# Performance work log

Hardware: AMD Instinct MI355X
Metric: run time of the kernel (lower is better)

Reference implementation:

```python
import jax, jax.numpy as jnp
import numpy as np

B, S, E = 2, 2048, 1024
H, D = 16, 64  # NUM_ATTENTION_HEADS, NUM_FEATURES
LN_EPS = 1e-5


def setup_inputs() -> dict:
    key = jax.random.key(0)
    ks = jax.random.split(key, 10)
    scale = 1.0 / np.sqrt(E)
    return {
        "x": jax.random.normal(ks[0], (B, S, E), dtype=jnp.float32),
        "ln_g": jnp.ones((E,), dtype=jnp.float32),
        "ln_b": jnp.zeros((E,), dtype=jnp.float32),
        "wq": jax.random.normal(ks[1], (E, H * D), dtype=jnp.float32) * scale,
        "bq": jnp.zeros((H * D,), dtype=jnp.float32),
        "wk": jax.random.normal(ks[2], (E, H * D), dtype=jnp.float32) * scale,
        "bk": jnp.zeros((H * D,), dtype=jnp.float32),
        "wv": jax.random.normal(ks[3], (E, H * D), dtype=jnp.float32) * scale,
        "bv": jnp.zeros((H * D,), dtype=jnp.float32),
        "wo": jax.random.normal(ks[4], (H * D, E), dtype=jnp.float32) * scale,
        "bo": jnp.zeros((E,), dtype=jnp.float32),
    }


def reference(x, ln_g, ln_b, wq, bq, wk, bk, wv, bv, wo, bo):
    x_residual = x
    # LayerNorm over last dim
    mean = jnp.mean(x, axis=-1, keepdims=True)
    var = jnp.mean(jnp.square(x - mean), axis=-1, keepdims=True)
    xn = (x - mean) * jax.lax.rsqrt(var + LN_EPS) * ln_g + ln_b

    q = (xn @ wq + bq).reshape(B, S, H, D)
    k = (xn @ wk + bk).reshape(B, S, H, D)
    v = (xn @ wv + bv).reshape(B, S, H, D)

    # scores: [B, S_q, S_k, H]
    score = jnp.einsum('bihd,bjhd->bijh', q, k) / np.sqrt(D).astype(np.float32)
    # causal mask: position i may not attend to j > i
    causal = jnp.tril(jnp.ones((S, S), dtype=bool))  # True = keep
    score = jnp.where(causal[None, :, :, None], score, -jnp.inf)
    probs = jax.nn.softmax(score, axis=2)

    out = jnp.einsum('bijh,bjhd->bihd', probs, v).reshape(B, S, H * D)
    out = out @ wo + bo
    return out + x_residual
```

## Files before the change

### kernel.cpp

```cpp
#include <hip/hip_runtime.h>
#include <math.h>
#include <stdint.h>

typedef short short8 __attribute__((ext_vector_type(8)));
typedef short s16x4 __attribute__((ext_vector_type(4)));
typedef float f32x4 __attribute__((ext_vector_type(4)));

constexpr int BB = 2, SS = 2048, EE = 1024, HH = 16, DD = 64, HD = 1024;
constexpr int NROW = BB * SS;
constexpr size_t WELEM = (size_t)1024 * 1024;
constexpr float LN_EPS = 1e-5f;

__device__ const int ENT_QT[40] = {0,1,2,3, 4,4, 5,5, 6,6, 7,7,
                                   8,8,8, 9,9,9, 10,10,10, 11,11,11,
                                   12,12,12,12, 13,13,13,13, 14,14,14,14, 15,15,15,15};
__device__ const int ENT_C0[40] = {0,0,0,0, 0,1, 0,1, 0,1, 0,1,
                                   0,1,2, 0,1,2, 0,1,2, 0,1,2,
                                   0,1,2,3, 0,1,2,3, 0,1,2,3, 0,1,2,3};
__device__ const int EBASE[16]  = {0,1,2,3,4,6,8,10,12,15,18,21,24,28,32,36};
constexpr int NENT = 40;

__device__ inline short f2bf(float f) {
    union { float f; uint32_t u; } v; v.f = f;
    uint32_t r = (v.u + 0x7fffu + ((v.u >> 16) & 1u)) >> 16;
    return (short)(uint16_t)r;
}

__device__ inline float bf2f(short s) {
    return __uint_as_float(((uint32_t)(uint16_t)s) << 16);
}

__device__ inline uint32_t pk2bf(float f0, float f1) {
    uint32_t u0 = __float_as_uint(f0) + 0x8000u;
    uint32_t u1 = __float_as_uint(f1) + 0x8000u;
    return __builtin_amdgcn_perm(u1, u0, 0x07060302u);
}

__device__ inline s16x4 pack_bf16x4(f32x4 v) {
    union { uint32_t u[2]; s16x4 s; } r;
    r.u[0] = pk2bf(v[0], v[1]);
    r.u[1] = pk2bf(v[2], v[3]);
    return r.s;
}

#define GLOBAL_TO_LDS16(g, l) \
    __builtin_amdgcn_global_load_lds( \
        (const __attribute__((address_space(1))) void*)(g), \
        (__attribute__((address_space(3))) void*)(l), 16, 0, 0)

__global__ void prep_kernel(const float* __restrict__ x,
                            const float* __restrict__ g,
                            const float* __restrict__ b,
                            short* __restrict__ xn,
                            const float* __restrict__ w0, const float* __restrict__ w1,
                            const float* __restrict__ w2, const float* __restrict__ w3,
                            short* __restrict__ wdst) {
    const int bx = blockIdx.x;
    const int t = threadIdx.x;
    if (bx < NROW) {
        const int row = bx;
        const float* xr = x + (size_t)row * EE;
        short* onr = xn + (size_t)row * EE;
        float4 v = ((const float4*)xr)[t];
        float s  = v.x + v.y + v.z + v.w;
        float ss = v.x * v.x + v.y * v.y + v.z * v.z + v.w * v.w;
        #pragma unroll
        for (int o = 32; o > 0; o >>= 1) {
            s  += __shfl_down(s, o);
            ss += __shfl_down(ss, o);
        }
        __shared__ float sm[4], sm2[4];
        const int wid = t >> 6, lane = t & 63;
        if (lane == 0) { sm[wid] = s; sm2[wid] = ss; }
        __syncthreads();
        float ts  = sm[0] + sm[1] + sm[2] + sm[3];
        float tss = sm2[0] + sm2[1] + sm2[2] + sm2[3];
        float mean = ts * (1.0f / EE);
        float var  = tss * (1.0f / EE) - mean * mean;
        float inv  = rsqrtf(var + LN_EPS);
        float4 gv = ((const float4*)g)[t];
        float4 bv = ((const float4*)b)[t];
        s16x4 st;
        st.x = f2bf((v.x - mean) * inv * gv.x + bv.x);
        st.y = f2bf((v.y - mean) * inv * gv.y + bv.y);
        st.z = f2bf((v.z - mean) * inv * gv.z + bv.z);
        st.w = f2bf((v.w - mean) * inv * gv.w + bv.w);
        ((s16x4*)onr)[t] = st;
    } else {
        const int widx = bx - NROW;
        const int z = widx >> 10;
        const int rem = widx & 1023;
        const int k0 = (rem >> 5) * 32, p0 = (rem & 31) * 32;
        const float* src = (z == 0) ? w0 : (z == 1) ? w1 : (z == 2) ? w2 : w3;
        short* d = wdst + (size_t)z * WELEM;
        __shared__ float tile[32][33];
        const int tx = t & 31, ty = t >> 5;
        #pragma unroll
        for (int r = ty; r < 32; r += 8)
            tile[r][tx] = src[(size_t)(k0 + r) * 1024 + p0 + tx];
        __syncthreads();
        #pragma unroll
        for (int r = ty; r < 32; r += 8)
            d[(size_t)(p0 + r) * 1024 + k0 + tx] = f2bf(tile[tx][r]);
    }
}

template <bool F32OUT>
__global__ __launch_bounds__(256) void mfma_gemm(
    const short* __restrict__ A,
    const short* __restrict__ BtBase,
    const float* __restrict__ b0, const float* __restrict__ b1,
    const float* __restrict__ b2,
    short* __restrict__ outB, short* __restrict__ outV,
    const float* __restrict__ resid, float* __restrict__ outF) {
    constexpr int K = 1024, N = 1024;
    const int t = threadIdx.x, lane = t & 63, w = t >> 6;
    const int quad = lane >> 4, l16 = lane & 15;
    const int wm = w >> 1, wn = w & 1;
    const int row0 = blockIdx.y * 128, col0 = blockIdx.x * 128;
    const int z = blockIdx.z;
    const short* Bt = BtBase + (size_t)z * WELEM;
    const float* bias = (z == 0) ? b0 : (z == 1) ? b1 : b2;

    __shared__ short As[128 * 32];
    __shared__ short Bs[128 * 32];

    f32x4 acc[4][4];
    #pragma unroll
    for (int i = 0; i < 4; i++)
        #pragma unroll
        for (int j = 0; j < 4; j++) acc[i][j] = (f32x4){0.f, 0.f, 0.f, 0.f};

    const int srow = t >> 2, schunk = t & 3;
    const short* agp = A  + (size_t)(row0 + srow) * K + schunk * 8;
    const short* bgp = Bt + (size_t)(col0 + srow) * K + schunk * 8;

    for (int k0 = 0; k0 < K; k0 += 32) {
        GLOBAL_TO_LDS16(agp + k0,                    As + t * 8);
        GLOBAL_TO_LDS16(agp + (size_t)64 * K + k0,   As + 2048 + t * 8);
        GLOBAL_TO_LDS16(bgp + k0,                    Bs + t * 8);
        GLOBAL_TO_LDS16(bgp + (size_t)64 * K + k0,   Bs + 2048 + t * 8);
        __syncthreads();
        short8 af[4], bf[4];
        #pragma unroll
        for (int mt = 0; mt < 4; mt++)
            af[mt] = *(const short8*)&As[(wm * 64 + mt * 16 + l16) * 32 + quad * 8];
        #pragma unroll
        for (int nt = 0; nt < 4; nt++)
            bf[nt] = *(const short8*)&Bs[(wn * 64 + nt * 16 + l16) * 32 + quad * 8];
        #pragma unroll
        for (int mt = 0; mt < 4; mt++)
            #pragma unroll
            for (int nt = 0; nt < 4; nt++)
                acc[mt][nt] = __builtin_amdgcn_mfma_f32_16x16x32_bf16(
                    af[mt], bf[nt], acc[mt][nt], 0, 0, 0);
        __syncthreads();
    }

    #pragma unroll
    for (int mt = 0; mt < 4; mt++) {
        #pragma unroll
        for (int nt = 0; nt < 4; nt++) {
            const int rbase = row0 + wm * 64 + mt * 16 + quad * 4;
            const int col = col0 + wn * 64 + nt * 16 + l16;
            const float bcol = bias[col];
            if (F32OUT) {
                #pragma unroll
                for (int r = 0; r < 4; r++)
                    outF[(size_t)(rbase + r) * N + col] =
                        acc[mt][nt][r] + bcol +
                        resid[(size_t)(rbase + r) * N + col];
            } else if (z == 2) {
                union { uint32_t u[2]; s16x4 s; } pk;
                pk.u[0] = pk2bf(acc[mt][nt][0] + bcol, acc[mt][nt][1] + bcol);
                pk.u[1] = pk2bf(acc[mt][nt][2] + bcol, acc[mt][nt][3] + bcol);
                *(s16x4*)&outV[(size_t)col * NROW + rbase] = pk.s;
            } else {
                #pragma unroll
                for (int r = 0; r < 4; r++)
                    outB[(size_t)z * NROW * N + (size_t)(rbase + r) * N + col] =
                        f2bf(acc[mt][nt][r] + bcol);
            }
        }
    }
}

__global__ __launch_bounds__(256) void attn_split(
    const short* __restrict__ q, const short* __restrict__ kkk,
    const short* __restrict__ vtp,
    short* __restrict__ OpartB, float* __restrict__ lpart) {
    const int e = NENT - 1 - (int)blockIdx.x;
    const int h = blockIdx.y, b = blockIdx.z;
    const int qt = ENT_QT[e], c0 = ENT_C0[e];
    const int t = threadIdx.x, lane = t & 63, w = t >> 6;
    const int quad = lane >> 4, l16 = lane & 15;
    const int sw = l16 & 7;
    const int i0 = qt * 128;

    __shared__ short Qs[128 * 64];
    __shared__ short Kb[2 * 64 * 64];
    __shared__ short Vb[2 * 64 * 64];

    const size_t qoff = ((size_t)(b * SS + i0)) * HD + h * DD;
    #pragma unroll
    for (int p = 0; p < 4; p++) {
        const int idx = t + p * 256;
        const int r = idx >> 3, cs = idx & 7;
        const int c = cs ^ (r & 7);
        GLOBAL_TO_LDS16(q + qoff + (size_t)r * HD + c * 8, Qs + idx * 8);
    }

    const int r0 = t >> 3,        cs0 = t & 7;
    const int r1 = (t + 256) >> 3, cs1 = (t + 256) & 7;
    const short* kb0 = kkk + ((size_t)b * SS) * HD + h * DD + (size_t)r0 * HD + (cs0 ^ (r0 & 7)) * 8;
    const short* kb1 = kkk + ((size_t)b * SS) * HD + h * DD + (size_t)r1 * HD + (cs1 ^ (r1 & 7)) * 8;
    const short* vb0 = vtp + ((size_t)(h * 64 + r0)) * NROW + b * SS + (cs0 ^ (r0 & 7)) * 8;
    const short* vb1 = vtp + ((size_t)(h * 64 + r1)) * NROW + b * SS + (cs1 ^ (r1 & 7)) * 8;

    f32x4 Ot[4][2];
    float lrun[2] = {0.f, 0.f};
    #pragma unroll
    for (int mtd = 0; mtd < 4; mtd++)
        #pragma unroll
        for (int nt = 0; nt < 2; nt++) Ot[mtd][nt] = (f32x4){0.f, 0.f, 0.f, 0.f};

    const int jt0 = c0 * 8;
    const int jt1 = min(jt0 + 8, 2 * qt + 2);

    {
        const size_t ko = (size_t)jt0 * 64 * HD;
        const int vo = jt0 * 64;
        GLOBAL_TO_LDS16(kb0 + ko, Kb + t * 8);
        GLOBAL_TO_LDS16(kb1 + ko, Kb + (t + 256) * 8);
        GLOBAL_TO_LDS16(vb0 + vo, Vb + t * 8);
        GLOBAL_TO_LDS16(vb1 + vo, Vb + (t + 256) * 8);
    }
    __syncthreads();

    int buf = 0;
    for (int jt = jt0; jt < jt1; ++jt) {
        if (jt + 1 < jt1) {
            const size_t ko = (size_t)(jt + 1) * 64 * HD;
            const int vo = (jt + 1) * 64;
            const int ob = (buf ^ 1) * 4096;
            GLOBAL_TO_LDS16(kb0 + ko, Kb + ob + t * 8);
            GLOBAL_TO_LDS16(kb1 + ko, Kb + ob + (t + 256) * 8);
            GLOBAL_TO_LDS16(vb0 + vo, Vb + ob + t * 8);
            GLOBAL_TO_LDS16(vb1 + vo, Vb + ob + (t + 256) * 8);
        }
        const short* Kc = Kb + buf * 4096;
        const short* Vc = Vb + buf * 4096;

        f32x4 s[4][2];
        #pragma unroll
        for (int mj = 0; mj < 4; mj++)
            #pragma unroll
            for (int nt = 0; nt < 2; nt++) s[mj][nt] = (f32x4){0.f, 0.f, 0.f, 0.f};
        #pragma unroll
        for (int ks = 0; ks < 2; ks++) {
            const int cq = ((ks * 4 + quad) ^ sw) * 8;
            short8 kf[4], qf[2];
            #pragma unroll
            for (int mj = 0; mj < 4; mj++)
                kf[mj] = *(const short8*)&Kc[(mj * 16 + l16) * 64 + cq];
            #pragma unroll
            for (int nt = 0; nt < 2; nt++)
                qf[nt] = *(const short8*)&Qs[(w * 32 + nt * 16 + l16) * 64 + cq];
            #pragma unroll
            for (int mj = 0; mj < 4; mj++)
                #pragma unroll
                for (int nt = 0; nt < 2; nt++)
                    s[mj][nt] = __builtin_amdgcn_mfma_f32_16x16x32_bf16(
                        kf[mj], qf[nt], s[mj][nt], 0, 0, 0);
        }

        const bool diag = (jt >= 2 * qt);
        const int joff = (jt - 2 * qt) * 64;
        const int irel = w * 32 + l16;
        #pragma unroll
        for (int mj = 0; mj < 4; mj++) {
            #pragma unroll
            for (int nt = 0; nt < 2; nt++) {
                const int ir = irel + nt * 16;
                #pragma unroll
                for (int r = 0; r < 4; r++) {
                    const int jrel = joff + mj * 16 + quad * 4 + r;
                    float p = exp2f(s[mj][nt][r] * 0.18033688f);
                    if (diag && (jrel > ir)) p = 0.f;
                    s[mj][nt][r] = p;
                    lrun[nt] += p;
                }
            }
        }

        #pragma unroll
        for (int ks2 = 0; ks2 < 4; ks2++) {
            s16x4 pf[2];
            #pragma unroll
            for (int nt = 0; nt < 2; nt++) pf[nt] = pack_bf16x4(s[ks2][nt]);
            #pragma unroll
            for (int mtd = 0; mtd < 4; mtd++) {
                const int cv = (((ks2 * 2 + (quad >> 1)) ^ sw) * 8) + (quad & 1) * 4;
                s16x4 vf = *(const s16x4*)&Vc[(mtd * 16 + l16) * 64 + cv];
                #pragma unroll
                for (int nt = 0; nt < 2; nt++)
                    Ot[mtd][nt] = __builtin_amdgcn_mfma_f32_16x16x16bf16_1k(
                        vf, pf[nt], Ot[mtd][nt], 0, 0, 0);
            }
        }
        __syncthreads();
        buf ^= 1;
    }

    const int slot = (b * HH + h) * NENT + e;
    #pragma unroll
    for (int nt = 0; nt < 2; nt++) {
        float l = lrun[nt];
        l += __shfl_xor(l, 16);
        l += __shfl_xor(l, 32);
        if (quad == 0) lpart[(size_t)slot * 128 + w * 32 + nt * 16 + l16] = l;
    }

    #pragma unroll
    for (int nt = 0; nt < 2; nt++) {
        const int i_rel = w * 32 + nt * 16 + l16;
        #pragma unroll
        for (int mtd = 0; mtd < 4; mtd++)
            *(s16x4*)&OpartB[(size_t)slot * 8192 + i_rel * 64 + mtd * 16 + quad * 4] =
                pack_bf16x4(Ot[mtd][nt]);
    }
}

__global__ __launch_bounds__(256) void attn_reduce(
    const short* __restrict__ OpartB, const float* __restrict__ lpart,
    short* __restrict__ attno) {
    const int qt = blockIdx.x, h = blockIdx.y, b = blockIdx.z;
    const int t = threadIdx.x;
    const int nch = (qt >> 2) + 1;
    const int slot0 = (b * HH + h) * NENT + EBASE[qt];
    const int i0 = qt * 128;
    #pragma unroll
    for (int it = 0; it < 8; it++) {
        const int g = t + it * 256;
        const int i = g >> 4, d4 = (g & 15) * 4;
        f32x4 acc = (f32x4){0.f, 0.f, 0.f, 0.f};
        float l = 0.f;
        for (int c = 0; c < nch; c++) {
            s16x4 pv = *(const s16x4*)&OpartB[(size_t)(slot0 + c) * 8192 + i * 64 + d4];
            acc[0] += bf2f(pv[0]);
            acc[1] += bf2f(pv[1]);
            acc[2] += bf2f(pv[2]);
            acc[3] += bf2f(pv[3]);
            l += lpart[(size_t)(slot0 + c) * 128 + i];
        }
        const float inv = 1.0f / l;
        union { uint32_t u[2]; s16x4 s; } pk;
        pk.u[0] = pk2bf(acc[0] * inv, acc[1] * inv);
        pk.u[1] = pk2bf(acc[2] * inv, acc[3] * inv);
        *(s16x4*)&attno[((size_t)(b * SS + i0 + i)) * HD + h * DD + d4] = pk.s;
    }
}

extern "C" void kernel_launch(void* const* d_in, const int* in_sizes, int n_in,
                              void* d_out, int out_size, void* d_ws, size_t ws_size,
                              hipStream_t stream) {
    const float* x    = (const float*)d_in[0];
    const float* ln_g = (const float*)d_in[1];
    const float* ln_b = (const float*)d_in[2];
    const float* wq   = (const float*)d_in[3];
    const float* bq   = (const float*)d_in[4];
    const float* wk   = (const float*)d_in[5];
    const float* bk   = (const float*)d_in[6];
    const float* wv   = (const float*)d_in[7];
    const float* bv   = (const float*)d_in[8];
    const float* wo   = (const float*)d_in[9];
    const float* bo   = (const float*)d_in[10];
    float* out = (float*)d_out;

    const size_t buf = (size_t)NROW * HD;
    short* xn    = (short*)d_ws;
    short* qb    = xn + buf;
    short* vt    = qb + 2 * buf;
    short* attno = vt + buf;
    short* wt    = attno + buf;
    short* OpB   = wt + 4 * WELEM;
    float* lpart = (float*)(OpB + (size_t)BB * HH * NENT * 8192);

    prep_kernel<<<2 * NROW, 256, 0, stream>>>(x, ln_g, ln_b, xn, wq, wk, wv, wo, wt);

    mfma_gemm<false><<<dim3(8, 32, 3), 256, 0, stream>>>(
        xn, wt, bq, bk, bv, qb, vt, nullptr, nullptr);

    attn_split<<<dim3(NENT, HH, BB), 256, 0, stream>>>(
        qb, qb + buf, vt, OpB, lpart);
    attn_reduce<<<dim3(16, HH, BB), 256, 0, stream>>>(OpB, lpart, attno);

    mfma_gemm<true><<<dim3(8, 32, 1), 256, 0, stream>>>(
        attno, wt + 3 * WELEM, bo, bo, bo, nullptr, nullptr, x, out);
}
```

Measured before the change: 222.0 us.

## Split attention loop into masked/unmasked phases, MFMA row sums, direct-write single-chunk tiles

Splits the key-tile loop into a mask-free main part and a diagonal part, so the causal-mask compare runs only on diagonal tiles. The softmax denominator is now accumulated with an extra MFMA against a ones vector instead of scalar adds plus cross-lane shuffles. Probabilities are packed to bf16 by truncation rather than rounding, and exp2 uses the hardware builtin. Query tiles with a single chunk (qt<4) normalize and write attention output directly, so the reduce kernel launches only for the remaining tiles. This trades some precision in P and adds MFMA work in exchange for fewer VALU ops and less partial-buffer traffic.

```diff
diff --git a/kernel.cpp b/kernel.cpp
--- a/kernel.cpp
+++ b/kernel.cpp
@@ -20,6 +20,15 @@
 __device__ const int EBASE[16]  = {0,1,2,3,4,6,8,10,12,15,18,21,24,28,32,36};
 constexpr int NENT = 40;
 
+#if defined(__has_builtin)
+#if __has_builtin(__builtin_amdgcn_exp2f)
+#define EXP2F(x) __builtin_amdgcn_exp2f(x)
+#endif
+#endif
+#ifndef EXP2F
+#define EXP2F(x) exp2f(x)
+#endif
+
 __device__ inline short f2bf(float f) {
     union { float f; uint32_t u; } v; v.f = f;
     uint32_t r = (v.u + 0x7fffu + ((v.u >> 16) & 1u)) >> 16;
@@ -34,6 +43,10 @@
     uint32_t u0 = __float_as_uint(f0) + 0x8000u;
     uint32_t u1 = __float_as_uint(f1) + 0x8000u;
     return __builtin_amdgcn_perm(u1, u0, 0x07060302u);
+}
+
+__device__ inline uint32_t pk2bf_t(float f0, float f1) {
+    return __builtin_amdgcn_perm(__float_as_uint(f1), __float_as_uint(f0), 0x07060302u);
 }
 
 __device__ inline s16x4 pack_bf16x4(f32x4 v) {
@@ -185,10 +198,90 @@
     }
 }
 
+#define ATTN_ITER(JT, DIAG)                                                     \
+    {                                                                           \
+        const int jt_ = (JT);                                                   \
+        if (jt_ + 1 < jt1) {                                                    \
+            const size_t ko = (size_t)(jt_ + 1) * 64 * HD;                      \
+            const int vo = (jt_ + 1) * 64;                                      \
+            const int ob = (buf ^ 1) * 4096;                                    \
+            GLOBAL_TO_LDS16(kb0 + ko, Kb + ob + t * 8);                         \
+            GLOBAL_TO_LDS16(kb1 + ko, Kb + ob + (t + 256) * 8);                 \
+            GLOBAL_TO_LDS16(vb0 + vo, Vb + ob + t * 8);                         \
+            GLOBAL_TO_LDS16(vb1 + vo, Vb + ob + (t + 256) * 8);                 \
+        }                                                                       \
+        const short* Kc = Kb + buf * 4096;                                      \
+        const short* Vc = Vb + buf * 4096;                                      \
+        f32x4 s[4][2];                                                          \
+        _Pragma("unroll")                                                       \
+        for (int mj = 0; mj < 4; mj++)                                          \
+            _Pragma("unroll")                                                   \
+            for (int nt = 0; nt < 2; nt++) s[mj][nt] = (f32x4){0.f,0.f,0.f,0.f};\
+        _Pragma("unroll")                                                       \
+        for (int ks = 0; ks < 2; ks++) {                                        \
+            const int cq = ((ks * 4 + quad) ^ sw) * 8;                          \
+            short8 kf[4], qf[2];                                                \
+            _Pragma("unroll")                                                   \
+            for (int mj = 0; mj < 4; mj++)                                      \
+                kf[mj] = *(const short8*)&Kc[(mj * 16 + l16) * 64 + cq];        \
+            _Pragma("unroll")                                                   \
+            for (int nt = 0; nt < 2; nt++)                                      \
+                qf[nt] = *(const short8*)&Qs[(w * 32 + nt * 16 + l16) * 64 + cq];\
+            _Pragma("unroll")                                                   \
+            for (int mj = 0; mj < 4; mj++)                                      \
+                _Pragma("unroll")                                               \
+                for (int nt = 0; nt < 2; nt++)                                  \
+                    s[mj][nt] = __builtin_amdgcn_mfma_f32_16x16x32_bf16(        \
+                        kf[mj], qf[nt], s[mj][nt], 0, 0, 0);                    \
+        }                                                                       \
+        const int joff = (jt_ - 2 * qt) * 64;                                   \
+        _Pragma("unroll")                                                       \
+        for (int mj = 0; mj < 4; mj++) {                                        \
+            _Pragma("unroll")                                                   \
+            for (int nt = 0; nt < 2; nt++) {                                    \
+                const int ir = irel + nt * 16;                                  \
+                _Pragma("unroll")                                               \
+                for (int r = 0; r < 4; r++) {                                   \
+                    float p = EXP2F(s[mj][nt][r] * 0.18033688f);                \
+                    if (DIAG) {                                                 \
+                        const int jrel = joff + mj * 16 + quad * 4 + r;         \
+                        if (jrel > ir) p = 0.f;                                 \
+                    }                                                           \
+                    s[mj][nt][r] = p;                                           \
+                }                                                               \
+            }                                                                   \
+        }                                                                       \
+        _Pragma("unroll")                                                       \
+        for (int ks2 = 0; ks2 < 4; ks2++) {                                     \
+            s16x4 pf[2];                                                        \
+            _Pragma("unroll")                                                   \
+            for (int nt = 0; nt < 2; nt++) {                                    \
+                union { uint32_t u[2]; s16x4 s4; } r_;                          \
+                r_.u[0] = pk2bf_t(s[ks2][nt][0], s[ks2][nt][1]);                \
+                r_.u[1] = pk2bf_t(s[ks2][nt][2], s[ks2][nt][3]);                \
+                pf[nt] = r_.s4;                                                 \
+                Lacc[nt] = __builtin_amdgcn_mfma_f32_16x16x16bf16_1k(           \
+                    onesf, pf[nt], Lacc[nt], 0, 0, 0);                          \
+            }                                                                   \
+            _Pragma("unroll")                                                   \
+            for (int mtd = 0; mtd < 4; mtd++) {                                 \
+                const int cv = (((ks2 * 2 + (quad >> 1)) ^ sw) * 8) + (quad & 1) * 4;\
+                s16x4 vf = *(const s16x4*)&Vc[(mtd * 16 + l16) * 64 + cv];      \
+                _Pragma("unroll")                                               \
+                for (int nt = 0; nt < 2; nt++)                                  \
+                    Ot[mtd][nt] = __builtin_amdgcn_mfma_f32_16x16x16bf16_1k(    \
+                        vf, pf[nt], Ot[mtd][nt], 0, 0, 0);                      \
+            }                                                                   \
+        }                                                                       \
+        __syncthreads();                                                        \
+        buf ^= 1;                                                               \
+    }
+
 __global__ __launch_bounds__(256) void attn_split(
     const short* __restrict__ q, const short* __restrict__ kkk,
     const short* __restrict__ vtp,
-    short* __restrict__ OpartB, float* __restrict__ lpart) {
+    short* __restrict__ OpartB, float* __restrict__ lpart,
+    short* __restrict__ attno) {
     const int e = NENT - 1 - (int)blockIdx.x;
     const int h = blockIdx.y, b = blockIdx.z;
     const int qt = ENT_QT[e], c0 = ENT_C0[e];
@@ -210,7 +303,7 @@
         GLOBAL_TO_LDS16(q + qoff + (size_t)r * HD + c * 8, Qs + idx * 8);
     }
 
-    const int r0 = t >> 3,        cs0 = t & 7;
+    const int r0 = t >> 3,         cs0 = t & 7;
     const int r1 = (t + 256) >> 3, cs1 = (t + 256) & 7;
     const short* kb0 = kkk + ((size_t)b * SS) * HD + h * DD + (size_t)r0 * HD + (cs0 ^ (r0 & 7)) * 8;
     const short* kb1 = kkk + ((size_t)b * SS) * HD + h * DD + (size_t)r1 * HD + (cs1 ^ (r1 & 7)) * 8;
@@ -218,14 +311,19 @@
     const short* vb1 = vtp + ((size_t)(h * 64 + r1)) * NROW + b * SS + (cs1 ^ (r1 & 7)) * 8;
 
     f32x4 Ot[4][2];
-    float lrun[2] = {0.f, 0.f};
+    f32x4 Lacc[2];
     #pragma unroll
     for (int mtd = 0; mtd < 4; mtd++)
         #pragma unroll
         for (int nt = 0; nt < 2; nt++) Ot[mtd][nt] = (f32x4){0.f, 0.f, 0.f, 0.f};
+    Lacc[0] = (f32x4){0.f, 0.f, 0.f, 0.f};
+    Lacc[1] = (f32x4){0.f, 0.f, 0.f, 0.f};
+    s16x4 onesf;
+    onesf[0] = onesf[1] = onesf[2] = onesf[3] = (short)0x3F80;
 
     const int jt0 = c0 * 8;
     const int jt1 = min(jt0 + 8, 2 * qt + 2);
+    const int irel = w * 32 + l16;
 
     {
         const size_t ko = (size_t)jt0 * 64 * HD;
@@ -238,103 +336,44 @@
     __syncthreads();
 
     int buf = 0;
-    for (int jt = jt0; jt < jt1; ++jt) {
-        if (jt + 1 < jt1) {
-            const size_t ko = (size_t)(jt + 1) * 64 * HD;
-            const int vo = (jt + 1) * 64;
-            const int ob = (buf ^ 1) * 4096;
-            GLOBAL_TO_LDS16(kb0 + ko, Kb + ob + t * 8);
-            GLOBAL_TO_LDS16(kb1 + ko, Kb + ob + (t + 256) * 8);
-            GLOBAL_TO_LDS16(vb0 + vo, Vb + ob + t * 8);
-            GLOBAL_TO_LDS16(vb1 + vo, Vb + ob + (t + 256) * 8);
-        }
-        const short* Kc = Kb + buf * 4096;
-        const short* Vc = Vb + buf * 4096;
-
-        f32x4 s[4][2];
-        #pragma unroll
-        for (int mj = 0; mj < 4; mj++)
+    const int dmid   = min(jt1, 2 * qt);
+    const int dstart = max(jt0, 2 * qt);
+    for (int jt = jt0; jt < dmid; ++jt) ATTN_ITER(jt, false)
+    for (int jt = dstart; jt < jt1; ++jt) ATTN_ITER(jt, true)
+
+    if (qt < 4) {
+        #pragma unroll
+        for (int nt = 0; nt < 2; nt++) {
+            const float inv = 1.0f / Lacc[nt][0];
+            const int i_abs = i0 + w * 32 + nt * 16 + l16;
+            const size_t ob = ((size_t)(b * SS + i_abs)) * HD + h * DD;
             #pragma unroll
-            for (int nt = 0; nt < 2; nt++) s[mj][nt] = (f32x4){0.f, 0.f, 0.f, 0.f};
-        #pragma unroll
-        for (int ks = 0; ks < 2; ks++) {
-            const int cq = ((ks * 4 + quad) ^ sw) * 8;
-            short8 kf[4], qf[2];
-            #pragma unroll
-            for (int mj = 0; mj < 4; mj++)
-                kf[mj] = *(const short8*)&Kc[(mj * 16 + l16) * 64 + cq];
-            #pragma unroll
-            for (int nt = 0; nt < 2; nt++)
-                qf[nt] = *(const short8*)&Qs[(w * 32 + nt * 16 + l16) * 64 + cq];
-            #pragma unroll
-            for (int mj = 0; mj < 4; mj++)
-                #pragma unroll
-                for (int nt = 0; nt < 2; nt++)
-                    s[mj][nt] = __builtin_amdgcn_mfma_f32_16x16x32_bf16(
-                        kf[mj], qf[nt], s[mj][nt], 0, 0, 0);
-        }
-
-        const bool diag = (jt >= 2 * qt);
-        const int joff = (jt - 2 * qt) * 64;
-        const int irel = w * 32 + l16;
-        #pragma unroll
-        for (int mj = 0; mj < 4; mj++) {
-            #pragma unroll
-            for (int nt = 0; nt < 2; nt++) {
-                const int ir = irel + nt * 16;
-                #pragma unroll
-                for (int r = 0; r < 4; r++) {
-                    const int jrel = joff + mj * 16 + quad * 4 + r;
-                    float p = exp2f(s[mj][nt][r] * 0.18033688f);
-                    if (diag && (jrel > ir)) p = 0.f;
-                    s[mj][nt][r] = p;
-                    lrun[nt] += p;
-                }
+            for (int mtd = 0; mtd < 4; mtd++) {
+                f32x4 val = Ot[mtd][nt];
+                union { uint32_t u[2]; s16x4 s4; } pk;
+                pk.u[0] = pk2bf(val[0] * inv, val[1] * inv);
+                pk.u[1] = pk2bf(val[2] * inv, val[3] * inv);
+                *(s16x4*)&attno[ob + mtd * 16 + quad * 4] = pk.s4;
             }
         }
-
-        #pragma unroll
-        for (int ks2 = 0; ks2 < 4; ks2++) {
-            s16x4 pf[2];
+    } else {
+        const int slot = (b * HH + h) * NENT + e;
+        #pragma unroll
+        for (int nt = 0; nt < 2; nt++) {
+            const int i_rel = w * 32 + nt * 16 + l16;
+            if (quad == 0) lpart[(size_t)slot * 128 + i_rel] = Lacc[nt][0];
             #pragma unroll
-            for (int nt = 0; nt < 2; nt++) pf[nt] = pack_bf16x4(s[ks2][nt]);
-            #pragma unroll
-            for (int mtd = 0; mtd < 4; mtd++) {
-                const int cv = (((ks2 * 2 + (quad >> 1)) ^ sw) * 8) + (quad & 1) * 4;
-                s16x4 vf = *(const s16x4*)&Vc[(mtd * 16 + l16) * 64 + cv];
-                #pragma unroll
-                for (int nt = 0; nt < 2; nt++)
-                    Ot[mtd][nt] = __builtin_amdgcn_mfma_f32_16x16x16bf16_1k(
-                        vf, pf[nt], Ot[mtd][nt], 0, 0, 0);
-            }
+            for (int mtd = 0; mtd < 4; mtd++)
+                *(s16x4*)&OpartB[(size_t)slot * 8192 + i_rel * 64 + mtd * 16 + quad * 4] =
+                    pack_bf16x4(Ot[mtd][nt]);
         }
-        __syncthreads();
-        buf ^= 1;
-    }
-
-    const int slot = (b * HH + h) * NENT + e;
-    #pragma unroll
-    for (int nt = 0; nt < 2; nt++) {
-        float l = lrun[nt];
-        l += __shfl_xor(l, 16);
-        l += __shfl_xor(l, 32);
-        if (quad == 0) lpart[(size_t)slot * 128 + w * 32 + nt * 16 + l16] = l;
-    }
-
-    #pragma unroll
-    for (int nt = 0; nt < 2; nt++) {
-        const int i_rel = w * 32 + nt * 16 + l16;
-        #pragma unroll
-        for (int mtd = 0; mtd < 4; mtd++)
-            *(s16x4*)&OpartB[(size_t)slot * 8192 + i_rel * 64 + mtd * 16 + quad * 4] =
-                pack_bf16x4(Ot[mtd][nt]);
     }
 }
 
 __global__ __launch_bounds__(256) void attn_reduce(
     const short* __restrict__ OpartB, const float* __restrict__ lpart,
     short* __restrict__ attno) {
-    const int qt = blockIdx.x, h = blockIdx.y, b = blockIdx.z;
+    const int qt = 4 + blockIdx.x, h = blockIdx.y, b = blockIdx.z;
     const int t = threadIdx.x;
     const int nch = (qt >> 2) + 1;
     const int slot0 = (b * HH + h) * NENT + EBASE[qt];
@@ -392,8 +431,8 @@
         xn, wt, bq, bk, bv, qb, vt, nullptr, nullptr);
 
     attn_split<<<dim3(NENT, HH, BB), 256, 0, stream>>>(
-        qb, qb + buf, vt, OpB, lpart);
-    attn_reduce<<<dim3(16, HH, BB), 256, 0, stream>>>(OpB, lpart, attno);
+        qb, qb + buf, vt, OpB, lpart, attno);
+    attn_reduce<<<dim3(12, HH, BB), 256, 0, stream>>>(OpB, lpart, attno);
 
     mfma_gemm<true><<<dim3(8, 32, 1), 256, 0, stream>>>(
         attno, wt + 3 * WELEM, bo, bo, bo, nullptr, nullptr, x, out);
```

Result: faster. 207.6 us (-6.5%).
